# Optimization experiments

Measured on AMD Instinct MI355X. Metric: run time of the kernel, lower is better.

The kernel has to match this reference:

```python
import jax, jax.numpy as jnp
import numpy as np

N = 50000      # nodes
E = 800000     # edges (avg degree 16)
D = 64         # hidden_dim == out_dim
L = 4          # number of GatedGCN layers
NB = 16        # num_bond_type
EPS_BN = 1e-5
EPS_ETA = 1e-6


def _bn(x, g, b):
    # training-mode batch norm over the node/edge axis
    mu = jnp.mean(x, axis=0, keepdims=True)
    var = jnp.var(x, axis=0, keepdims=True)
    return (x - mu) * jax.lax.rsqrt(var + EPS_BN) * g + b


def setup_inputs() -> dict:
    key = jax.random.key(0)
    ks = iter(jax.random.split(key, 64))
    s = 0.05

    def w(shape):
        return jax.random.normal(next(ks), shape, dtype=jnp.float32) * s

    inp = {
        "h_ids": jax.random.randint(next(ks), (N,), 0, N),
        "e_ids": jax.random.randint(next(ks), (E,), 0, NB),
        "f_ids": jax.random.randint(next(ks), (N,), 0, N),
        "src": jax.random.randint(next(ks), (E,), 0, N),
        "dst": jax.random.randint(next(ks), (E,), 0, N),
        "emb_h": w((N, D)),
        "emb_e": w((NB, D)),
        "emb_f": w((N, D)),
        "A1_w": w((L, D, D)), "A1_b": jnp.zeros((L, D), jnp.float32),
        "A2_w": w((L, 2 * D, D)), "A2_b": jnp.zeros((L, D), jnp.float32),
        "B1_w": w((L, D, D)), "B1_b": jnp.zeros((L, D), jnp.float32),
        "B2_w": w((L, D, D)), "B2_b": jnp.zeros((L, D), jnp.float32),
        "B3_w": w((L, D, D)), "B3_b": jnp.zeros((L, D), jnp.float32),
        "C1_w": w((L, D, D)), "C1_b": jnp.zeros((L, D), jnp.float32),
        "C2_w": w((L, D, D)), "C2_b": jnp.zeros((L, D), jnp.float32),
        "bn_h_g": jnp.ones((L, D), jnp.float32), "bn_h_b": jnp.zeros((L, D), jnp.float32),
        "bn_e_g": jnp.ones((L, D), jnp.float32), "bn_e_b": jnp.zeros((L, D), jnp.float32),
        "mlp_w0": w((D, D // 2)), "mlp_b0": jnp.zeros((D // 2,), jnp.float32),
        "mlp_w1": w((D // 2, D // 4)), "mlp_b1": jnp.zeros((D // 4,), jnp.float32),
        "mlp_w2": w((D // 4, 1)), "mlp_b2": jnp.zeros((1,), jnp.float32),
    }
    return inp


def reference(h_ids, e_ids, f_ids, src, dst,
              emb_h, emb_e, emb_f,
              A1_w, A1_b, A2_w, A2_b, B1_w, B1_b, B2_w, B2_b, B3_w, B3_b,
              C1_w, C1_b, C2_w, C2_b,
              bn_h_g, bn_h_b, bn_e_g, bn_e_b,
              mlp_w0, mlp_b0, mlp_w1, mlp_b1, mlp_w2, mlp_b2):
    h = emb_h[h_ids]          # [N, D]
    e = emb_e[e_ids]          # [E, D]
    p = emb_f[f_ids]          # [N, D]

    seg = lambda m: jax.ops.segment_sum(m, dst, num_segments=N)

    for i in range(L):
        h_in, e_in, p_in = h, e, p
        # per-node projections (dense GEMMs), then irregular gathers per edge
        B1h = h @ B1_w[i] + B1_b[i]
        B2h = h @ B2_w[i] + B2_b[i]
        B3e = e @ B3_w[i] + B3_b[i]
        hat_eta = B1h[src] + B2h[dst] + B3e           # [E, D]
        sigma = jax.nn.sigmoid(hat_eta)
        sum_sigma = seg(sigma)                        # [N, D] scatter-sum at dst
        eta = sigma / (sum_sigma[dst] + EPS_ETA)      # [E, D]

        v = jnp.concatenate([h, p], axis=-1) @ A2_w[i] + A2_b[i]  # [N, D]
        sum_eta_v = seg(eta * v[src])
        h_new = h @ A1_w[i] + A1_b[i] + sum_eta_v

        C2p = p @ C2_w[i] + C2_b[i]
        sum_eta_p = seg(eta * C2p[src])
        p_new = p @ C1_w[i] + C1_b[i] + sum_eta_p

        h = jax.nn.relu(_bn(h_new, bn_h_g[i], bn_h_b[i]))
        e_new = jax.nn.relu(_bn(hat_eta, bn_e_g[i], bn_e_b[i]))
        p = jnp.tanh(p_new)
        # residual (input_dim == output_dim in every layer)
        h = h_in + h
        e = e_in + e_new
        p = p_in + p

    hg = jnp.mean(h, axis=0)  # mean readout over the (single) graph -> [D]
    y = jax.nn.relu(hg @ mlp_w0 + mlp_b0)
    y = jax.nn.relu(y @ mlp_w1 + mlp_b1)
    y = y @ mlp_w2 + mlp_b2   # [1]
    return y
```

## Files before the change

### kernel.cpp

```cpp
#include <hip/hip_runtime.h>
#include <math.h>

#define NN 50000
#define EE 800000
#define LL 4

typedef unsigned short u16;
typedef unsigned int u32;
typedef __attribute__((ext_vector_type(8))) short bf16x8;
typedef __attribute__((ext_vector_type(4))) float f32x4;

__device__ __forceinline__ float rlane(float v, int l) {
  return __int_as_float(__builtin_amdgcn_readlane(__float_as_int(v), l));
}

__device__ __forceinline__ float matvec64(float xv, const float* __restrict__ w) {
  float a0 = 0.f, a1 = 0.f, a2 = 0.f, a3 = 0.f;
#pragma unroll
  for (int k = 0; k < 64; k += 4) {
    a0 = fmaf(rlane(xv, k + 0), w[k + 0], a0);
    a1 = fmaf(rlane(xv, k + 1), w[k + 1], a1);
    a2 = fmaf(rlane(xv, k + 2), w[k + 2], a2);
    a3 = fmaf(rlane(xv, k + 3), w[k + 3], a3);
  }
  return (a0 + a1) + (a2 + a3);
}

__device__ __forceinline__ float sigm(float x) { return 1.f / (1.f + __expf(-x)); }

__device__ __forceinline__ u16 f2b(float x) {
  u32 u = __float_as_uint(x);
  u32 r = (u + 0x7FFFu + ((u >> 16) & 1u)) >> 16;
  return (u16)r;
}
__device__ __forceinline__ float b2f(u16 b) { return __uint_as_float(((u32)b) << 16); }

struct FragA { bf16x8 hi0, hi1, lo0, lo1; };

__device__ __forceinline__ void load_a(const float* __restrict__ base, int l, FragA& fa) {
  const int row = l & 15, quad = l >> 4;
  const float* src = base + (size_t)row * 64 + quad * 8;
  bf16x8 h0, h1, l0, l1;
#pragma unroll
  for (int j = 0; j < 8; ++j) {
    float x0 = src[j], x1 = src[32 + j];
    u16 a0 = f2b(x0), a1 = f2b(x1);
    h0[j] = (short)a0; h1[j] = (short)a1;
    l0[j] = (short)f2b(x0 - b2f(a0));
    l1[j] = (short)f2b(x1 - b2f(a1));
  }
  fa.hi0 = h0; fa.hi1 = h1; fa.lo0 = l0; fa.lo1 = l1;
}

__device__ __forceinline__ void gemm_acc(const FragA& fa, const float* __restrict__ W,
                                         int l, f32x4 acc[4]) {
  const int row = l & 15, quad = l >> 4;
#pragma unroll
  for (int cb = 0; cb < 4; ++cb) {
    f32x4 z = acc[cb];
#pragma unroll
    for (int kb = 0; kb < 2; ++kb) {
      bf16x8 bhi, blo;
      const float* wp = W + (size_t)(kb * 32 + quad * 8) * 64 + cb * 16 + row;
#pragma unroll
      for (int j = 0; j < 8; ++j) {
        float wv = wp[(size_t)j * 64];
        u16 aa = f2b(wv);
        bhi[j] = (short)aa;
        blo[j] = (short)f2b(wv - b2f(aa));
      }
      const bf16x8 ahi = kb ? fa.hi1 : fa.hi0;
      const bf16x8 alo = kb ? fa.lo1 : fa.lo0;
      z = __builtin_amdgcn_mfma_f32_16x16x32_bf16(ahi, bhi, z, 0, 0, 0);
      z = __builtin_amdgcn_mfma_f32_16x16x32_bf16(alo, bhi, z, 0, 0, 0);
      z = __builtin_amdgcn_mfma_f32_16x16x32_bf16(ahi, blo, z, 0, 0, 0);
    }
    acc[cb] = z;
  }
}

__device__ __forceinline__ void store16(const f32x4 acc[4], const float* __restrict__ bias,
                                        int l, float* __restrict__ out) {
  const int row = l & 15, quad = l >> 4;
#pragma unroll
  for (int cb = 0; cb < 4; ++cb) {
    int col = cb * 16 + row;
    float bv = bias[col];
#pragma unroll
    for (int r = 0; r < 4; ++r)
      out[(size_t)(quad * 4 + r) * 64 + col] = acc[cb][r] + bv;
  }
}

__global__ void k_t2(const float* __restrict__ h, const float* __restrict__ B1w,
                     int* __restrict__ flag) {
  int l = threadIdx.x;
  FragA fa;
  load_a(h, l, fa);
  f32x4 acc[4];
  acc[0] = (f32x4){0,0,0,0}; acc[1] = (f32x4){0,0,0,0};
  acc[2] = (f32x4){0,0,0,0}; acc[3] = (f32x4){0,0,0,0};
  gemm_acc(fa, B1w, l, acc);
  const int row = l & 15, quad = l >> 4;
  int ok = 1;
#pragma unroll
  for (int cb = 0; cb < 4; ++cb)
#pragma unroll
    for (int r = 0; r < 4; ++r) {
      int nrow = quad * 4 + r, col = cb * 16 + row;
      float ref = 0.f;
      for (int k = 0; k < 64; ++k) ref += h[nrow * 64 + k] * B1w[k * 64 + col];
      if (fabsf(acc[cb][r] - ref) > 3e-3f + 3e-3f * fabsf(ref)) ok = 0;
    }
  ok = __all(ok);
  if (l == 0) flag[0] = ok;
}

__global__ void k_hist(const int* __restrict__ dst, int* __restrict__ counts) {
  int i = blockIdx.x * 256 + threadIdx.x;
  if (i < EE) atomicAdd(&counts[dst[i]], 1);
}

__global__ void k_scan(const int* __restrict__ counts, int* __restrict__ row_start,
                       int* __restrict__ cursor) {
  __shared__ int sd[1024];
  int tid = threadIdx.x;
  int running = 0;
  for (int basei = 0; basei < NN; basei += 1024) {
    int i = basei + tid;
    int v = (i < NN) ? counts[i] : 0;
    sd[tid] = v;
    __syncthreads();
    for (int ofs = 1; ofs < 1024; ofs <<= 1) {
      int t = (tid >= ofs) ? sd[tid - ofs] : 0;
      __syncthreads();
      sd[tid] += t;
      __syncthreads();
    }
    int incl = sd[tid];
    int total = sd[1023];
    if (i < NN) { int e = running + incl - v; row_start[i] = e; cursor[i] = e; }
    running += total;
    __syncthreads();
  }
  if (tid == 0) row_start[NN] = EE;
}

__global__ void k_scatter(const int* __restrict__ dst, const int* __restrict__ src,
                          const int* __restrict__ e_ids,
                          int* __restrict__ cursor, int* __restrict__ src_s,
                          int* __restrict__ eids_s) {
  int i = blockIdx.x * 256 + threadIdx.x;
  if (i < EE) {
    int d = dst[i];
    int pos = atomicAdd(&cursor[d], 1);
    src_s[pos] = src[i];
    eids_s[pos] = e_ids[i];
  }
}

__global__ void k_einit(const int* __restrict__ eids_s, const float* __restrict__ emb_e,
                        u16* __restrict__ e_sorted) {
  int idx = blockIdx.x * 256 + threadIdx.x;
  if (idx >= EE * 64) return;
  int ed = idx >> 6, f = idx & 63;
  e_sorted[idx] = f2b(emb_e[eids_s[ed] * 64 + f]);
}

__global__ void k_ninit(const int* __restrict__ h_ids, const int* __restrict__ f_ids,
                        const float* __restrict__ emb_h, const float* __restrict__ emb_f,
                        float* __restrict__ h, float* __restrict__ p) {
  int idx = blockIdx.x * 256 + threadIdx.x;
  if (idx >= NN * 64) return;
  int n = idx >> 6, f = idx & 63;
  h[idx] = emb_h[h_ids[n] * 64 + f];
  p[idx] = emb_f[f_ids[n] * 64 + f];
}

__global__ void __launch_bounds__(256) k_Am(
    int mode,
    float* __restrict__ h, float* __restrict__ p,
    float* __restrict__ hn, float* __restrict__ pn,
    const float* __restrict__ mu_h, const float* __restrict__ ir_h,
    const float* __restrict__ g_h, const float* __restrict__ b_h,
    const float* __restrict__ B1w, const float* __restrict__ B1b,
    const float* __restrict__ B2w, const float* __restrict__ B2b,
    const float* __restrict__ A1w, const float* __restrict__ A1b,
    const float* __restrict__ C1w, const float* __restrict__ C1b,
    const float* __restrict__ C2w, const float* __restrict__ C2b,
    const float* __restrict__ A2w, const float* __restrict__ A2b,
    float* __restrict__ B1h, float* __restrict__ B2h,
    float* __restrict__ vbuf, float* __restrict__ C2p,
    const int* __restrict__ flag) {
  if (!flag[0]) return;
  const int f = threadIdx.x & 63;
  const int wv = threadIdx.x >> 6;
  const int base0 = (blockIdx.x * 4 + wv) * 16;
  if (base0 >= NN) return;

  if (mode) {
    float mu = mu_h[f], ir = ir_h[f], ga = g_h[f], be = b_h[f];
    for (int i = 0; i < 16; ++i) {
      int n = base0 + i;
      float hv = hn[(size_t)n * 64 + f];
      h[(size_t)n * 64 + f] += fmaxf(0.f, (hv - mu) * ir * ga + be);
      float pv = pn[(size_t)n * 64 + f];
      p[(size_t)n * 64 + f] += tanhf(pv);
    }
  }

  FragA fh, fq;
  load_a(h + (size_t)base0 * 64, f, fh);
  load_a(p + (size_t)base0 * 64, f, fq);
  f32x4 acc[4];
#define ZERO4 { acc[0]=(f32x4){0,0,0,0}; acc[1]=(f32x4){0,0,0,0}; \
                acc[2]=(f32x4){0,0,0,0}; acc[3]=(f32x4){0,0,0,0}; }
  ZERO4; gemm_acc(fh, B1w, f, acc); store16(acc, B1b, f, B1h + (size_t)base0 * 64);
  ZERO4; gemm_acc(fh, B2w, f, acc); store16(acc, B2b, f, B2h + (size_t)base0 * 64);
  ZERO4; gemm_acc(fh, A1w, f, acc); store16(acc, A1b, f, hn + (size_t)base0 * 64);
  ZERO4; gemm_acc(fq, C1w, f, acc); store16(acc, C1b, f, pn + (size_t)base0 * 64);
  ZERO4; gemm_acc(fq, C2w, f, acc); store16(acc, C2b, f, C2p + (size_t)base0 * 64);
  ZERO4; gemm_acc(fh, A2w, f, acc); gemm_acc(fq, A2w + 4096, f, acc);
  store16(acc, A2b, f, vbuf + (size_t)base0 * 64);
#undef ZERO4
}

__global__ void __launch_bounds__(256) k_Av(
    int mode,
    float* __restrict__ h, float* __restrict__ p,
    float* __restrict__ hn, float* __restrict__ pn,
    const float* __restrict__ mu_h, const float* __restrict__ ir_h,
    const float* __restrict__ g_h, const float* __restrict__ b_h,
    const float* __restrict__ B1w, const float* __restrict__ B1b,
    const float* __restrict__ B2w, const float* __restrict__ B2b,
    const float* __restrict__ A1w, const float* __restrict__ A1b,
    const float* __restrict__ C1w, const float* __restrict__ C1b,
    const float* __restrict__ C2w, const float* __restrict__ C2b,
    const float* __restrict__ A2w, const float* __restrict__ A2b,
    float* __restrict__ B1h, float* __restrict__ B2h,
    float* __restrict__ vbuf, float* __restrict__ C2p,
    const int* __restrict__ flag) {
  if (flag[0]) return;
  const int f = threadIdx.x & 63;
  const int wv = threadIdx.x >> 6;
  const int base0 = (blockIdx.x * 4 + wv) * 16;
  if (base0 >= NN) return;

  if (mode) {
    float mu = mu_h[f], ir = ir_h[f], ga = g_h[f], be = b_h[f];
    for (int i = 0; i < 16; ++i) {
      int n = base0 + i;
      float hv = hn[n * 64 + f];
      h[n * 64 + f] += fmaxf(0.f, (hv - mu) * ir * ga + be);
      float pv = pn[n * 64 + f];
      p[n * 64 + f] += tanhf(pv);
    }
  }

  float w[64];
#define LOADW(WP) _Pragma("unroll") for (int k = 0; k < 64; ++k) w[k] = (WP)[k * 64 + f];
  LOADW(B1w);
  { float bb = B1b[f];
    for (int i = 0; i < 16; ++i) { int n = base0 + i;
      B1h[n * 64 + f] = matvec64(h[n * 64 + f], w) + bb; } }
  LOADW(B2w);
  { float bb = B2b[f];
    for (int i = 0; i < 16; ++i) { int n = base0 + i;
      B2h[n * 64 + f] = matvec64(h[n * 64 + f], w) + bb; } }
  LOADW(A1w);
  { float bb = A1b[f];
    for (int i = 0; i < 16; ++i) { int n = base0 + i;
      hn[n * 64 + f] = matvec64(h[n * 64 + f], w) + bb; } }
  LOADW(C1w);
  { float bb = C1b[f];
    for (int i = 0; i < 16; ++i) { int n = base0 + i;
      pn[n * 64 + f] = matvec64(p[n * 64 + f], w) + bb; } }
  LOADW(C2w);
  { float bb = C2b[f];
    for (int i = 0; i < 16; ++i) { int n = base0 + i;
      C2p[n * 64 + f] = matvec64(p[n * 64 + f], w) + bb; } }
  {
    float w2[64];
#pragma unroll
    for (int k = 0; k < 64; ++k) { w[k] = A2w[k * 64 + f]; w2[k] = A2w[(k + 64) * 64 + f]; }
    float bb = A2b[f];
    for (int i = 0; i < 16; ++i) { int n = base0 + i;
      vbuf[n * 64 + f] = matvec64(h[n * 64 + f], w) + matvec64(p[n * 64 + f], w2) + bb; }
  }
#undef LOADW
}

template <int SH>
__global__ void __launch_bounds__(256) k_B(
    const u16* __restrict__ e_sorted, const float* __restrict__ B1h,
    const float* __restrict__ B2h, const int* __restrict__ src_s,
    const int* __restrict__ row_start,
    const float* __restrict__ B3w, const float* __restrict__ B3b,
    u16* __restrict__ hat, float* __restrict__ sum_sigma,
    float* __restrict__ eS1, float* __restrict__ eS2) {
  const int f = threadIdx.x & 63;
  const int wv = threadIdx.x >> 6;
  const int nb = (blockIdx.x * 4 + wv) * 4;
  if (nb >= NN) return;
  float w[64];
#pragma unroll
  for (int k = 0; k < 64; ++k) w[k] = B3w[k * 64 + f];
  float bb = B3b[f];
  float s1 = 0.f, s2 = 0.f;
  for (int i = 0; i < 4; ++i) {
    int n = nb + i;
    float b2 = B2h[n * 64 + f];
    float ssum = 0.f;
    int t0 = row_start[n], t1 = row_start[n + 1];
    for (int t = t0; t < t1; ++t) {
      float xv = b2f(e_sorted[t * 64 + f]);
      int s = src_s[t];
      float acc = matvec64(xv, w) + bb + b2 + B1h[s * 64 + f];
      if (SH) {
        u16 hb = f2b(acc);
        hat[t * 64 + f] = hb;
        acc = b2f(hb);
      }
      float sg = sigm(acc);
      ssum += sg; s1 += acc; s2 += acc * acc;
    }
    sum_sigma[n * 64 + f] = ssum;
  }
  int slot = (blockIdx.x & 255) * 64 + f;
  atomicAdd(&eS1[slot], s1);
  atomicAdd(&eS2[slot], s2);
}

__global__ void k_red(const float* __restrict__ S1, const float* __restrict__ S2,
                      float cnt, float* __restrict__ mu, float* __restrict__ ir) {
  int f = threadIdx.x;
  float a = 0.f, b = 0.f;
  for (int j = 0; j < 256; ++j) { a += S1[j * 64 + f]; b += S2[j * 64 + f]; }
  float m = a / cnt;
  float var = fmaxf(b / cnt - m * m, 0.f);
  mu[f] = m;
  ir[f] = rsqrtf(var + 1e-5f);
}

template <int SH, int LAST>
__global__ void __launch_bounds__(256) k_C(
    const u16* __restrict__ hat, u16* __restrict__ e_sorted,
    const float* __restrict__ B1h, const float* __restrict__ B2h,
    const float* __restrict__ B3w, const float* __restrict__ B3b,
    const float* __restrict__ vbuf, const float* __restrict__ C2p,
    const int* __restrict__ src_s, const int* __restrict__ row_start,
    const float* __restrict__ sum_sigma,
    float* __restrict__ hn, float* __restrict__ pn,
    const float* __restrict__ mu_e, const float* __restrict__ ir_e,
    const float* __restrict__ g_e, const float* __restrict__ b_e,
    float* __restrict__ hS1, float* __restrict__ hS2) {
  const int f = threadIdx.x & 63;
  const int wv = threadIdx.x >> 6;
  const int n = blockIdx.x * 4 + wv;
  if (n >= NN) return;
  float w[64];
  float bb = 0.f;
  if (!SH) {
#pragma unroll
    for (int k = 0; k < 64; ++k) w[k] = B3w[k * 64 + f];
    bb = B3b[f];
  }
  float mu = mu_e[f], ir = ir_e[f], ga = g_e[f], be = b_e[f];
  float inv = 1.f / (sum_sigma[n * 64 + f] + 1e-6f);
  float ahv = 0.f, ahp = 0.f;
  int t0 = row_start[n], t1 = row_start[n + 1];
  int t = t0;
  if (SH) {
    for (; t + 4 <= t1; t += 4) {
      int s0 = src_s[t + 0] * 64, s1 = src_s[t + 1] * 64;
      int s2 = src_s[t + 2] * 64, s3 = src_s[t + 3] * 64;
      float hv0 = b2f(hat[(size_t)(t + 0) * 64 + f]);
      float hv1 = b2f(hat[(size_t)(t + 1) * 64 + f]);
      float hv2 = b2f(hat[(size_t)(t + 2) * 64 + f]);
      float hv3 = b2f(hat[(size_t)(t + 3) * 64 + f]);
      float v0 = vbuf[s0 + f], v1 = vbuf[s1 + f], v2 = vbuf[s2 + f], v3 = vbuf[s3 + f];
      float et0 = sigm(hv0) * inv, et1 = sigm(hv1) * inv;
      float et2 = sigm(hv2) * inv, et3 = sigm(hv3) * inv;
      ahv += et0 * v0 + et1 * v1 + et2 * v2 + et3 * v3;
      if (!LAST) {
        float ev0 = b2f(e_sorted[(size_t)(t + 0) * 64 + f]);
        float ev1 = b2f(e_sorted[(size_t)(t + 1) * 64 + f]);
        float ev2 = b2f(e_sorted[(size_t)(t + 2) * 64 + f]);
        float ev3 = b2f(e_sorted[(size_t)(t + 3) * 64 + f]);
        float c0 = C2p[s0 + f], c1 = C2p[s1 + f], c2 = C2p[s2 + f], c3 = C2p[s3 + f];
        ahp += et0 * c0 + et1 * c1 + et2 * c2 + et3 * c3;
        e_sorted[(size_t)(t + 0) * 64 + f] = f2b(ev0 + fmaxf(0.f, (hv0 - mu) * ir * ga + be));
        e_sorted[(size_t)(t + 1) * 64 + f] = f2b(ev1 + fmaxf(0.f, (hv1 - mu) * ir * ga + be));
        e_sorted[(size_t)(t + 2) * 64 + f] = f2b(ev2 + fmaxf(0.f, (hv2 - mu) * ir * ga + be));
        e_sorted[(size_t)(t + 3) * 64 + f] = f2b(ev3 + fmaxf(0.f, (hv3 - mu) * ir * ga + be));
      }
    }
  }
  for (; t < t1; ++t) {
    int s = src_s[t] * 64;
    float ev = 0.f;
    if (!SH || !LAST) ev = b2f(e_sorted[(size_t)t * 64 + f]);
    float hatv;
    if (SH) hatv = b2f(hat[(size_t)t * 64 + f]);
    else    hatv = matvec64(ev, w) + bb + B2h[n * 64 + f] + B1h[s + f];
    float eta = sigm(hatv) * inv;
    ahv = fmaf(eta, vbuf[s + f], ahv);
    if (!LAST) {
      ahp = fmaf(eta, C2p[s + f], ahp);
      e_sorted[(size_t)t * 64 + f] = f2b(ev + fmaxf(0.f, (hatv - mu) * ir * ga + be));
    }
  }
  float hv = hn[n * 64 + f] + ahv; hn[n * 64 + f] = hv;
  if (!LAST) pn[n * 64 + f] += ahp;
  int slot = (blockIdx.x & 255) * 64 + f;
  atomicAdd(&hS1[slot], hv);
  atomicAdd(&hS2[slot], hv * hv);
}

__global__ void __launch_bounds__(256) k_F1(
    const float* __restrict__ hn, const float* __restrict__ h,
    const float* __restrict__ mu, const float* __restrict__ ir,
    const float* __restrict__ ga, const float* __restrict__ be,
    float* __restrict__ hsum) {
  int f = threadIdx.x & 63, wv = threadIdx.x >> 6;
  float m = mu[f], r = ir[f], g = ga[f], b = be[f];
  float ps = 0.f;
  for (int n = blockIdx.x * 4 + wv; n < NN; n += gridDim.x * 4)
    ps += h[n * 64 + f] + fmaxf(0.f, (hn[n * 64 + f] - m) * r * g + b);
  atomicAdd(&hsum[f], ps);
}

__global__ void k_F2(const float* __restrict__ hsum,
                     const float* __restrict__ w0, const float* __restrict__ b0,
                     const float* __restrict__ w1, const float* __restrict__ b1,
                     const float* __restrict__ w2, const float* __restrict__ b2,
                     float* __restrict__ out) {
  __shared__ float hg[64]; __shared__ float y0[32]; __shared__ float y1[16];
  int t = threadIdx.x;
  hg[t] = hsum[t] * (1.f / (float)NN);
  __syncthreads();
  if (t < 32) { float a = b0[t];
    for (int k = 0; k < 64; ++k) a = fmaf(hg[k], w0[k * 32 + t], a);
    y0[t] = fmaxf(a, 0.f); }
  __syncthreads();
  if (t < 16) { float a = b1[t];
    for (int k = 0; k < 32; ++k) a = fmaf(y0[k], w1[k * 16 + t], a);
    y1[t] = fmaxf(a, 0.f); }
  __syncthreads();
  if (t == 0) { float a = b2[0];
    for (int k = 0; k < 16; ++k) a = fmaf(y1[k], w2[k], a);
    out[0] = a; }
}

__global__ void k_report(float* out, float v) { out[0] = v; }

extern "C" void kernel_launch(void* const* d_in, const int* in_sizes, int n_in,
                              void* d_out, int out_size, void* d_ws, size_t ws_size,
                              hipStream_t stream) {
  (void)in_sizes; (void)n_in; (void)out_size;
  const int* h_ids = (const int*)d_in[0];
  const int* e_ids = (const int*)d_in[1];
  const int* f_ids = (const int*)d_in[2];
  const int* src   = (const int*)d_in[3];
  const int* dst   = (const int*)d_in[4];
  const float* emb_h = (const float*)d_in[5];
  const float* emb_e = (const float*)d_in[6];
  const float* emb_f = (const float*)d_in[7];
  const float* A1_w = (const float*)d_in[8];  const float* A1_b = (const float*)d_in[9];
  const float* A2_w = (const float*)d_in[10]; const float* A2_b = (const float*)d_in[11];
  const float* B1_w = (const float*)d_in[12]; const float* B1_b = (const float*)d_in[13];
  const float* B2_w = (const float*)d_in[14]; const float* B2_b = (const float*)d_in[15];
  const float* B3_w = (const float*)d_in[16]; const float* B3_b = (const float*)d_in[17];
  const float* C1_w = (const float*)d_in[18]; const float* C1_b = (const float*)d_in[19];
  const float* C2_w = (const float*)d_in[20]; const float* C2_b = (const float*)d_in[21];
  const float* bn_h_g = (const float*)d_in[22]; const float* bn_h_b = (const float*)d_in[23];
  const float* bn_e_g = (const float*)d_in[24]; const float* bn_e_b = (const float*)d_in[25];
  const float* mlp_w0 = (const float*)d_in[26]; const float* mlp_b0 = (const float*)d_in[27];
  const float* mlp_w1 = (const float*)d_in[28]; const float* mlp_b1 = (const float*)d_in[29];
  const float* mlp_w2 = (const float*)d_in[30]; const float* mlp_b2 = (const float*)d_in[31];

  auto pad = [](size_t b) { return (b + 255) & ~(size_t)255; };
  const size_t sz_e    = pad((size_t)EE * 64 * 2);
  const size_t sz_node = pad((size_t)NN * 64 * 4);
  const size_t sz_cnt  = pad((size_t)NN * 4);
  const size_t sz_row  = pad((size_t)(NN + 1) * 4);
  const size_t sz_ei   = pad((size_t)EE * 4);
  const size_t sz_stat = pad((size_t)LL * 2 * 256 * 64 * 4);
  const size_t sz_vec  = pad(64 * 4);

  size_t base_need = sz_e + 9 * sz_node + 2 * sz_cnt + sz_row + 2 * sz_ei +
                     2 * sz_stat + 6 * sz_vec;
  bool store_hat = (base_need + sz_e) <= ws_size;
  if (base_need > ws_size) {
    k_report<<<1, 1, 0, stream>>>((float*)d_out, (float)(ws_size >> 20) + 0.125f);
    return;
  }

  char* cur = (char*)d_ws;
  auto alloc = [&](size_t bytes) -> char* { char* r = cur; cur += bytes; return r; };
  u16* e_sorted = (u16*)alloc(sz_e);
  u16* hat      = store_hat ? (u16*)alloc(sz_e) : (u16*)e_sorted;
  float* h    = (float*)alloc(sz_node);
  float* p    = (float*)alloc(sz_node);
  float* hn   = (float*)alloc(sz_node);
  float* pn   = (float*)alloc(sz_node);
  float* B1h  = (float*)alloc(sz_node);
  float* B2h  = (float*)alloc(sz_node);
  float* vbuf = (float*)alloc(sz_node);
  float* C2p  = (float*)alloc(sz_node);
  float* ssig = (float*)alloc(sz_node);
  int* counts    = (int*)alloc(sz_cnt);
  int* cursor    = (int*)alloc(sz_cnt);
  int* row_start = (int*)alloc(sz_row);
  int* src_s     = (int*)alloc(sz_ei);
  int* eids_s    = (int*)alloc(sz_ei);
  float* estats = (float*)alloc(sz_stat);
  float* hstats = (float*)alloc(sz_stat);
  float* hsum   = (float*)alloc(sz_vec);
  float* mu_h = (float*)alloc(sz_vec);
  float* ir_h = (float*)alloc(sz_vec);
  float* mu_e = (float*)alloc(sz_vec);
  float* ir_e = (float*)alloc(sz_vec);
  int* flag  = (int*)alloc(sz_vec);

  hipMemsetAsync(counts, 0, sz_cnt, stream);
  hipMemsetAsync(estats, 0, 2 * sz_stat + sz_vec, stream);

  k_hist<<<(EE + 255) / 256, 256, 0, stream>>>(dst, counts);
  k_scan<<<1, 1024, 0, stream>>>(counts, row_start, cursor);
  k_scatter<<<(EE + 255) / 256, 256, 0, stream>>>(dst, src, e_ids, cursor, src_s, eids_s);
  k_einit<<<(EE * 64) / 256, 256, 0, stream>>>(eids_s, emb_e, e_sorted);
  k_ninit<<<(NN * 64 + 255) / 256, 256, 0, stream>>>(h_ids, f_ids, emb_h, emb_f, h, p);
  k_t2<<<1, 64, 0, stream>>>(h, B1_w, flag);

  const int STAT = 2 * 256 * 64;
  for (int i = 0; i < LL; ++i) {
    if (i > 0) {
      k_red<<<1, 64, 0, stream>>>(hstats + (i - 1) * STAT,
                                  hstats + (i - 1) * STAT + 256 * 64, (float)NN, mu_h, ir_h);
    }
    const float* gh = bn_h_g + (i > 0 ? (i - 1) * 64 : 0);
    const float* bh = bn_h_b + (i > 0 ? (i - 1) * 64 : 0);
    k_Am<<<(NN + 63) / 64, 256, 0, stream>>>(
        (i > 0) ? 1 : 0, h, p, hn, pn, mu_h, ir_h, gh, bh,
        B1_w + i * 4096, B1_b + i * 64, B2_w + i * 4096, B2_b + i * 64,
        A1_w + i * 4096, A1_b + i * 64, C1_w + i * 4096, C1_b + i * 64,
        C2_w + i * 4096, C2_b + i * 64, A2_w + i * 8192, A2_b + i * 64,
        B1h, B2h, vbuf, C2p, flag);
    k_Av<<<(NN + 63) / 64, 256, 0, stream>>>(
        (i > 0) ? 1 : 0, h, p, hn, pn, mu_h, ir_h, gh, bh,
        B1_w + i * 4096, B1_b + i * 64, B2_w + i * 4096, B2_b + i * 64,
        A1_w + i * 4096, A1_b + i * 64, C1_w + i * 4096, C1_b + i * 64,
        C2_w + i * 4096, C2_b + i * 64, A2_w + i * 8192, A2_b + i * 64,
        B1h, B2h, vbuf, C2p, flag);
    if (store_hat)
      k_B<1><<<(NN + 15) / 16, 256, 0, stream>>>(
          e_sorted, B1h, B2h, src_s, row_start, B3_w + i * 4096, B3_b + i * 64,
          hat, ssig, estats + i * STAT, estats + i * STAT + 256 * 64);
    else
      k_B<0><<<(NN + 15) / 16, 256, 0, stream>>>(
          e_sorted, B1h, B2h, src_s, row_start, B3_w + i * 4096, B3_b + i * 64,
          hat, ssig, estats + i * STAT, estats + i * STAT + 256 * 64);
    k_red<<<1, 64, 0, stream>>>(estats + i * STAT, estats + i * STAT + 256 * 64,
                                (float)EE, mu_e, ir_e);
    bool lastL = (i == LL - 1);
    if (store_hat) {
      if (lastL)
        k_C<1, 1><<<(NN + 3) / 4, 256, 0, stream>>>(
            hat, e_sorted, B1h, B2h, B3_w + i * 4096, B3_b + i * 64, vbuf, C2p,
            src_s, row_start, ssig, hn, pn, mu_e, ir_e,
            bn_e_g + i * 64, bn_e_b + i * 64,
            hstats + i * STAT, hstats + i * STAT + 256 * 64);
      else
        k_C<1, 0><<<(NN + 3) / 4, 256, 0, stream>>>(
            hat, e_sorted, B1h, B2h, B3_w + i * 4096, B3_b + i * 64, vbuf, C2p,
            src_s, row_start, ssig, hn, pn, mu_e, ir_e,
            bn_e_g + i * 64, bn_e_b + i * 64,
            hstats + i * STAT, hstats + i * STAT + 256 * 64);
    } else {
      k_C<0, 0><<<(NN + 3) / 4, 256, 0, stream>>>(
          hat, e_sorted, B1h, B2h, B3_w + i * 4096, B3_b + i * 64, vbuf, C2p,
          src_s, row_start, ssig, hn, pn, mu_e, ir_e,
          bn_e_g + i * 64, bn_e_b + i * 64,
          hstats + i * STAT, hstats + i * STAT + 256 * 64);
    }
  }
  k_red<<<1, 64, 0, stream>>>(hstats + 3 * STAT, hstats + 3 * STAT + 256 * 64,
                              (float)NN, mu_h, ir_h);
  k_F1<<<512, 256, 0, stream>>>(hn, h, mu_h, ir_h, bn_h_g + 3 * 64, bn_h_b + 3 * 64, hsum);
  k_F2<<<1, 64, 0, stream>>>(hsum, mlp_w0, mlp_b0, mlp_w1, mlp_b1, mlp_w2, mlp_b2,
                             (float*)d_out);
}
```

Before: 2.389 ms.

## Defer edge residual update from k_C into next layer's k_B

The edge-feature residual update (e += relu(BN(hat_eta))) moves out of the aggregation kernel k_C and into the next layer's k_B. k_B now reads the previous layer's stored hat, applies BN, ReLU and the residual, and writes the result back, except in the last layer where it only uses it locally. This removes a separate read-modify-write pass over e_sorted in k_C and skips the final layer's edge update and its stats reduction entirely. In exchange k_B does extra reads, and the mu_e/ir_e buffers must still hold the previous layer's stats when k_B runs.

```diff
diff --git a/kernel.cpp b/kernel.cpp
--- a/kernel.cpp
+++ b/kernel.cpp
@@ -290,12 +290,14 @@
 #undef LOADW
 }
 
-template <int SH>
+template <int SH, int MODE>
 __global__ void __launch_bounds__(256) k_B(
-    const u16* __restrict__ e_sorted, const float* __restrict__ B1h,
+    u16* __restrict__ e_sorted, const float* __restrict__ B1h,
     const float* __restrict__ B2h, const int* __restrict__ src_s,
     const int* __restrict__ row_start,
     const float* __restrict__ B3w, const float* __restrict__ B3b,
+    const float* __restrict__ mu_p, const float* __restrict__ ir_p,
+    const float* __restrict__ g_p, const float* __restrict__ b_p,
     u16* __restrict__ hat, float* __restrict__ sum_sigma,
     float* __restrict__ eS1, float* __restrict__ eS2) {
   const int f = threadIdx.x & 63;
@@ -306,6 +308,8 @@
 #pragma unroll
   for (int k = 0; k < 64; ++k) w[k] = B3w[k * 64 + f];
   float bb = B3b[f];
+  float mu = 0.f, ir = 0.f, ga = 0.f, be = 0.f;
+  if (MODE >= 1) { mu = mu_p[f]; ir = ir_p[f]; ga = g_p[f]; be = b_p[f]; }
   float s1 = 0.f, s2 = 0.f;
   for (int i = 0; i < 4; ++i) {
     int n = nb + i;
@@ -313,12 +317,18 @@
     float ssum = 0.f;
     int t0 = row_start[n], t1 = row_start[n + 1];
     for (int t = t0; t < t1; ++t) {
-      float xv = b2f(e_sorted[t * 64 + f]);
+      float xv = b2f(e_sorted[(size_t)t * 64 + f]);
+      if (MODE >= 1) {
+        float pv = b2f(hat[(size_t)t * 64 + f]);
+        u16 q = f2b(xv + fmaxf(0.f, (pv - mu) * ir * ga + be));
+        if (MODE == 1) e_sorted[(size_t)t * 64 + f] = q;
+        xv = b2f(q);
+      }
       int s = src_s[t];
       float acc = matvec64(xv, w) + bb + b2 + B1h[s * 64 + f];
       if (SH) {
         u16 hb = f2b(acc);
-        hat[t * 64 + f] = hb;
+        hat[(size_t)t * 64 + f] = hb;
         acc = b2f(hb);
       }
       float sg = sigm(acc);
@@ -383,23 +393,15 @@
       float et2 = sigm(hv2) * inv, et3 = sigm(hv3) * inv;
       ahv += et0 * v0 + et1 * v1 + et2 * v2 + et3 * v3;
       if (!LAST) {
-        float ev0 = b2f(e_sorted[(size_t)(t + 0) * 64 + f]);
-        float ev1 = b2f(e_sorted[(size_t)(t + 1) * 64 + f]);
-        float ev2 = b2f(e_sorted[(size_t)(t + 2) * 64 + f]);
-        float ev3 = b2f(e_sorted[(size_t)(t + 3) * 64 + f]);
         float c0 = C2p[s0 + f], c1 = C2p[s1 + f], c2 = C2p[s2 + f], c3 = C2p[s3 + f];
         ahp += et0 * c0 + et1 * c1 + et2 * c2 + et3 * c3;
-        e_sorted[(size_t)(t + 0) * 64 + f] = f2b(ev0 + fmaxf(0.f, (hv0 - mu) * ir * ga + be));
-        e_sorted[(size_t)(t + 1) * 64 + f] = f2b(ev1 + fmaxf(0.f, (hv1 - mu) * ir * ga + be));
-        e_sorted[(size_t)(t + 2) * 64 + f] = f2b(ev2 + fmaxf(0.f, (hv2 - mu) * ir * ga + be));
-        e_sorted[(size_t)(t + 3) * 64 + f] = f2b(ev3 + fmaxf(0.f, (hv3 - mu) * ir * ga + be));
       }
     }
   }
   for (; t < t1; ++t) {
     int s = src_s[t] * 64;
     float ev = 0.f;
-    if (!SH || !LAST) ev = b2f(e_sorted[(size_t)t * 64 + f]);
+    if (!SH) ev = b2f(e_sorted[(size_t)t * 64 + f]);
     float hatv;
     if (SH) hatv = b2f(hat[(size_t)t * 64 + f]);
     else    hatv = matvec64(ev, w) + bb + B2h[n * 64 + f] + B1h[s + f];
@@ -407,7 +409,8 @@
     ahv = fmaf(eta, vbuf[s + f], ahv);
     if (!LAST) {
       ahp = fmaf(eta, C2p[s + f], ahp);
-      e_sorted[(size_t)t * 64 + f] = f2b(ev + fmaxf(0.f, (hatv - mu) * ir * ga + be));
+      if (!SH)
+        e_sorted[(size_t)t * 64 + f] = f2b(ev + fmaxf(0.f, (hatv - mu) * ir * ga + be));
     }
   }
   float hv = hn[n * 64 + f] + ahv; hn[n * 64 + f] = hv;
@@ -534,6 +537,7 @@
   k_t2<<<1, 64, 0, stream>>>(h, B1_w, flag);
 
   const int STAT = 2 * 256 * 64;
+  const int GB = (NN + 15) / 16, GC = (NN + 3) / 4;
   for (int i = 0; i < LL; ++i) {
     if (i > 0) {
       k_red<<<1, 64, 0, stream>>>(hstats + (i - 1) * STAT,
@@ -553,32 +557,49 @@
         A1_w + i * 4096, A1_b + i * 64, C1_w + i * 4096, C1_b + i * 64,
         C2_w + i * 4096, C2_b + i * 64, A2_w + i * 8192, A2_b + i * 64,
         B1h, B2h, vbuf, C2p, flag);
-    if (store_hat)
-      k_B<1><<<(NN + 15) / 16, 256, 0, stream>>>(
+    const float* gp = bn_e_g + (i > 0 ? (i - 1) * 64 : 0);
+    const float* bp = bn_e_b + (i > 0 ? (i - 1) * 64 : 0);
+    if (store_hat) {
+      if (i == 0)
+        k_B<1, 0><<<GB, 256, 0, stream>>>(
+            e_sorted, B1h, B2h, src_s, row_start, B3_w + i * 4096, B3_b + i * 64,
+            mu_e, ir_e, gp, bp, hat, ssig,
+            estats + i * STAT, estats + i * STAT + 256 * 64);
+      else if (i < LL - 1)
+        k_B<1, 1><<<GB, 256, 0, stream>>>(
+            e_sorted, B1h, B2h, src_s, row_start, B3_w + i * 4096, B3_b + i * 64,
+            mu_e, ir_e, gp, bp, hat, ssig,
+            estats + i * STAT, estats + i * STAT + 256 * 64);
+      else
+        k_B<1, 2><<<GB, 256, 0, stream>>>(
+            e_sorted, B1h, B2h, src_s, row_start, B3_w + i * 4096, B3_b + i * 64,
+            mu_e, ir_e, gp, bp, hat, ssig,
+            estats + i * STAT, estats + i * STAT + 256 * 64);
+    } else {
+      k_B<0, 0><<<GB, 256, 0, stream>>>(
           e_sorted, B1h, B2h, src_s, row_start, B3_w + i * 4096, B3_b + i * 64,
-          hat, ssig, estats + i * STAT, estats + i * STAT + 256 * 64);
-    else
-      k_B<0><<<(NN + 15) / 16, 256, 0, stream>>>(
-          e_sorted, B1h, B2h, src_s, row_start, B3_w + i * 4096, B3_b + i * 64,
-          hat, ssig, estats + i * STAT, estats + i * STAT + 256 * 64);
-    k_red<<<1, 64, 0, stream>>>(estats + i * STAT, estats + i * STAT + 256 * 64,
-                                (float)EE, mu_e, ir_e);
+          mu_e, ir_e, gp, bp, hat, ssig,
+          estats + i * STAT, estats + i * STAT + 256 * 64);
+    }
+    if (!store_hat || i < LL - 1)
+      k_red<<<1, 64, 0, stream>>>(estats + i * STAT, estats + i * STAT + 256 * 64,
+                                  (float)EE, mu_e, ir_e);
     bool lastL = (i == LL - 1);
     if (store_hat) {
       if (lastL)
-        k_C<1, 1><<<(NN + 3) / 4, 256, 0, stream>>>(
+        k_C<1, 1><<<GC, 256, 0, stream>>>(
             hat, e_sorted, B1h, B2h, B3_w + i * 4096, B3_b + i * 64, vbuf, C2p,
             src_s, row_start, ssig, hn, pn, mu_e, ir_e,
             bn_e_g + i * 64, bn_e_b + i * 64,
             hstats + i * STAT, hstats + i * STAT + 256 * 64);
       else
-        k_C<1, 0><<<(NN + 3) / 4, 256, 0, stream>>>(
+        k_C<1, 0><<<GC, 256, 0, stream>>>(
             hat, e_sorted, B1h, B2h, B3_w + i * 4096, B3_b + i * 64, vbuf, C2p,
             src_s, row_start, ssig, hn, pn, mu_e, ir_e,
             bn_e_g + i * 64, bn_e_b + i * 64,
             hstats + i * STAT, hstats + i * STAT + 256 * 64);
     } else {
-      k_C<0, 0><<<(NN + 3) / 4, 256, 0, stream>>>(
+      k_C<0, 0><<<GC, 256, 0, stream>>>(
           hat, e_sorted, B1h, B2h, B3_w + i * 4096, B3_b + i * 64, vbuf, C2p,
           src_s, row_start, ssig, hn, pn, mu_e, ir_e,
           bn_e_g + i * 64, bn_e_b + i * 64,
```

Measured after the change: 2.393 ms. About the same (+0.1%).
